# Optimization experiments

Measured on AMD Instinct MI355X. Metric: run time of the kernel, lower is better.

Reference implementation:

```python
import jax, jax.numpy as jnp
import numpy as np

N, C, P, M = 8, 20, 8732, 16
THRESHOLD, NEG_POS_RATIO, ALPHA = 0.5, 3, 1.0


def cxcy_to_xy(c):
    return jnp.concatenate([c[..., :2] - c[..., 2:] / 2.0, c[..., :2] + c[..., 2:] / 2.0], axis=-1)


def xy_to_cxcy(xy):
    return jnp.concatenate([(xy[..., :2] + xy[..., 2:]) / 2.0, xy[..., 2:] - xy[..., :2]], axis=-1)


def cxcy_to_gcxgcy(cxcy, priors):
    g_cxcy = (cxcy[..., :2] - priors[..., :2]) / (priors[..., 2:] / 10.0)
    g_wh = jnp.log(cxcy[..., 2:] / priors[..., 2:]) * 5.0
    return jnp.concatenate([g_cxcy, g_wh], axis=-1)


def jaccard(a, b):
    # a: (M,4), b: (P,4), boundary coords -> IoU (M,P)
    lo = jnp.maximum(a[:, None, :2], b[None, :, :2])
    hi = jnp.minimum(a[:, None, 2:], b[None, :, 2:])
    inter = jnp.prod(jnp.clip(hi - lo, 0.0), axis=-1)
    area_a = jnp.prod(a[:, 2:] - a[:, :2], axis=-1)
    area_b = jnp.prod(b[:, 2:] - b[:, :2], axis=-1)
    return inter / (area_a[:, None] + area_b[None, :] - inter)


def setup_inputs() -> dict:
    key = jax.random.key(0)
    k1, k2, k3, k4, k5, k6 = jax.random.split(key, 6)
    predicted_locs = jax.random.normal(k1, (N, C, P, 4), jnp.float32)
    predicted_scores = jax.random.normal(k2, (N, C, P, 2), jnp.float32)
    # valid ground-truth boundary boxes (x1<x2, y1<y2) in [0,1]
    ctr = jax.random.uniform(k3, (N, C, M, 2), minval=0.2, maxval=0.8)
    wh = jax.random.uniform(k4, (N, C, M, 2), minval=0.05, maxval=0.3)
    boxes = jnp.concatenate([ctr - wh / 2.0, ctr + wh / 2.0], axis=-1)
    # valid priors in cxcywh (w,h > 0 so log-encoding is finite)
    pctr = jax.random.uniform(k5, (P, 2), minval=0.05, maxval=0.95)
    pwh = jax.random.uniform(k6, (P, 2), minval=0.05, maxval=0.5)
    priors_cxcy = jnp.concatenate([pctr, pwh], axis=-1)
    labels = jnp.ones((N, C, M), jnp.int32)  # binary per-class head: object label = 1
    return {
        "predicted_locs": predicted_locs,
        "predicted_scores": predicted_scores,
        "boxes": boxes,
        "labels": labels,
        "priors_cxcy": priors_cxcy,
    }


def _forward(predicted_locs, predicted_scores, boxes, priors_cxcy, labels):
    n_classes = predicted_scores.shape[1]
    n_priors = predicted_scores.shape[2]
    priors_xy = cxcy_to_xy(priors_cxcy)

    def match(b, lab):
        # b: (M,4) boundary, lab: (M,) int
        ov = jaccard(b, priors_xy)                       # (M,P)
        obj_for_prior = jnp.argmax(ov, axis=0)           # (P,)
        ov_for_prior = jnp.max(ov, axis=0)               # (P,)
        prior_for_obj = jnp.argmax(ov, axis=1)           # (M,)
        # force each object to own its best prior
        obj_for_prior = obj_for_prior.at[prior_for_obj].set(jnp.arange(b.shape[0]))
        ov_for_prior = ov_for_prior.at[prior_for_obj].set(1.0)
        cls = jnp.where(ov_for_prior < THRESHOLD, 0, lab[obj_for_prior])  # (P,)
        tl = cxcy_to_gcxgcy(xy_to_cxcy(b[obj_for_prior]), priors_cxcy)    # (P,4)
        return tl, cls

    true_locs, true_classes = jax.vmap(jax.vmap(match))(boxes, labels)  # (N,C,P,4), (N,C,P)

    pos = true_classes != 0                      # (N,C,P)
    posf = pos.astype(predicted_locs.dtype)
    n_pos_bc = posf.sum(axis=2)                  # (N,C) positives per image per class
    n_pos_c = n_pos_bc.sum(axis=0)               # (C,)

    # localization: mean L1 over positive priors (4 coords each), per class
    l1 = jnp.abs(predicted_locs - true_locs).sum(-1) * posf   # (N,C,P)
    loc_loss_c = l1.sum(axis=(0, 2)) / jnp.maximum(n_pos_c * 4.0, 1.0)

    # per-prior binary cross entropy
    logp = jax.nn.log_softmax(predicted_scores, axis=-1)      # (N,C,P,2)
    ce = -jnp.take_along_axis(logp, true_classes[..., None], axis=-1)[..., 0]  # (N,C,P)
    conf_pos_c = (ce * posf).sum(axis=(0, 2))

    # hard negative mining: sort negatives desc per (image,class) row, keep top 3*n_pos
    ce_neg = jnp.where(pos, 0.0, ce)
    ce_neg_sorted = -jnp.sort(-ce_neg, axis=-1)               # (N,C,P) descending
    n_hard = NEG_POS_RATIO * n_pos_bc                         # (N,C)
    ranks = jnp.arange(n_priors, dtype=n_hard.dtype)
    hard_mask = ranks[None, None, :] < n_hard[..., None]
    conf_hard_c = (ce_neg_sorted * hard_mask).sum(axis=(0, 2))

    safe = jnp.maximum(n_pos_c, 1.0)
    loss_c = jnp.where(
        n_pos_c > 0,
        (conf_pos_c + conf_hard_c + ALPHA * loc_loss_c) / safe,
        0.0,
    ) / n_classes
    return loss_c.sum()


def reference(predicted_locs, predicted_scores, boxes, labels, priors_cxcy):
    return _forward(predicted_locs, predicted_scores, boxes, priors_cxcy, labels)
```

## Files before the change

### kernel.cpp

```cpp
#include <hip/hip_runtime.h>
#include <math.h>

#define NN 8
#define CC 20
#define PP 8732
#define MM 16
#define NPR 3
#define SPLIT 8
#define CH 1092
#define ROWS (NN * CC)

__device__ __forceinline__ float fast_rcp(float x) { return __builtin_amdgcn_rcpf(x); }

__device__ __forceinline__ float lse2(float a, float b) {
    float mx = fmaxf(a, b);
    float d  = fabsf(a - b);
    return mx + logf(1.0f + expf(-d));
}

#define ABLK 256
__global__ __launch_bounds__(ABLK) void mbox_p1(
    const float* __restrict__ locs, const float* __restrict__ scores,
    const float* __restrict__ boxes, const int* __restrict__ labels,
    const float* __restrict__ priors,
    unsigned char* __restrict__ pk8, float* __restrict__ ce0,
    unsigned long long* __restrict__ partials, float* __restrict__ cstats)
{
    const int row = blockIdx.x >> 3;
    const int chunk = blockIdx.x & 7;
    const int tid = threadIdx.x, lane = tid & 63, wav = tid >> 6;
    __shared__ float s_bx1[MM], s_by1[MM], s_bx2[MM], s_by2[MM], s_area[MM];
    __shared__ float s_bcx[MM], s_bcy[MM], s_bw[MM], s_bh[MM];
    __shared__ int s_lab[MM];
    __shared__ unsigned long long s_pk[4 * MM];
    __shared__ float s_rf[4 * 3];

    if (tid < MM) {
        const float* b = boxes + ((size_t)row * MM + tid) * 4;
        float x1 = b[0], y1 = b[1], x2 = b[2], y2 = b[3];
        s_bx1[tid] = x1; s_by1[tid] = y1; s_bx2[tid] = x2; s_by2[tid] = y2;
        s_area[tid] = (x2 - x1) * (y2 - y1);
        s_bcx[tid] = (x1 + x2) * 0.5f; s_bcy[tid] = (y1 + y2) * 0.5f;
        s_bw[tid] = x2 - x1; s_bh[tid] = y2 - y1;
        s_lab[tid] = labels[row * MM + tid];
    }
    __syncthreads();

    const float4* pri4 = (const float4*)priors;
    const float4* loc4 = (const float4*)(locs + (size_t)row * PP * 4);
    const float2* sc2  = (const float2*)(scores + (size_t)row * PP * 2);
    unsigned char* pk  = pk8 + (size_t)row * PP;
    float* cer         = ce0 + (size_t)row * PP;

    float bestv[MM]; int bestp[MM];
#pragma unroll
    for (int m = 0; m < MM; m++) { bestv[m] = -1.0f; bestp[m] = 0x7fffffff; }
    float l_np = 0.0f, l_l1 = 0.0f, l_cp = 0.0f;
    const int p0 = chunk * CH, p1e = min(p0 + CH, PP);

    for (int p = p0 + tid; p < p1e; p += ABLK) {
        float4 pr = pri4[p];
        float hw = pr.z * 0.5f, hh = pr.w * 0.5f;
        float px1 = pr.x - hw, py1 = pr.y - hh;
        float px2 = pr.x + hw, py2 = pr.y + hh;
        float area_b = (px2 - px1) * (py2 - py1);
        float bov = -1.0f; int bm = 0;
#pragma unroll
        for (int m = 0; m < MM; m++) {
            float dx = fminf(s_bx2[m], px2) - fmaxf(s_bx1[m], px1);
            float dy = fminf(s_by2[m], py2) - fmaxf(s_by1[m], py1);
            dx = fmaxf(dx, 0.0f); dy = fmaxf(dy, 0.0f);
            float inter = dx * dy;
            float den = s_area[m] + area_b - inter;
            float iou = inter * fast_rcp(den);
            if (iou > bov) { bov = iou; bm = m; }
            if (iou > bestv[m]) { bestv[m] = iou; bestp[m] = p; }
        }
        float2 sc = sc2[p];
        float lse = lse2(sc.x, sc.y);
        bool pos = (bov >= 0.5f) && (s_lab[bm] != 0);
        pk[p]  = (unsigned char)((pos ? 16u : 0u) | (unsigned)bm);
        cer[p] = pos ? 0.0f : fmaxf(lse - sc.x, 0.0f);
        if (pos) {
            l_np += 1.0f;
            l_cp += lse - sc.y;
            float4 pl = loc4[p];
            float tx = (s_bcx[bm] - pr.x) * 10.0f / pr.z;
            float ty = (s_bcy[bm] - pr.y) * 10.0f / pr.w;
            float tw = logf(s_bw[bm] / pr.z) * 5.0f;
            float th = logf(s_bh[bm] / pr.w) * 5.0f;
            l_l1 += fabsf(pl.x - tx) + fabsf(pl.y - ty) + fabsf(pl.z - tw) + fabsf(pl.w - th);
        }
    }

#pragma unroll
    for (int m = 0; m < MM; m++) {
        unsigned long long key =
            ((unsigned long long)__float_as_uint(bestv[m]) << 32) |
            (unsigned)(0x7fffffff - bestp[m]);
#pragma unroll
        for (int off = 32; off; off >>= 1) {
            unsigned long long o = __shfl_down(key, off);
            if (o > key) key = o;
        }
        if (lane == 0) s_pk[wav * MM + m] = key;
    }
#pragma unroll
    for (int off = 32; off; off >>= 1) {
        l_np += __shfl_down(l_np, off);
        l_l1 += __shfl_down(l_l1, off);
        l_cp += __shfl_down(l_cp, off);
    }
    if (lane == 0) { s_rf[wav * 3] = l_np; s_rf[wav * 3 + 1] = l_l1; s_rf[wav * 3 + 2] = l_cp; }
    __syncthreads();
    if (tid < MM) {
        unsigned long long key = s_pk[tid];
        for (int w = 1; w < 4; w++) {
            unsigned long long o = s_pk[w * MM + tid];
            if (o > key) key = o;
        }
        partials[((size_t)row * MM + tid) * SPLIT + chunk] = key;
    }
    if (tid == 0) {
        float np = 0, l1 = 0, cp = 0;
        for (int w = 0; w < 4; w++) { np += s_rf[w * 3]; l1 += s_rf[w * 3 + 1]; cp += s_rf[w * 3 + 2]; }
        float* cs = cstats + ((size_t)row * SPLIT + chunk) * 3;
        cs[0] = np; cs[1] = l1; cs[2] = cp;
    }
}

#define CBLK 1024
#define EPT 9
__global__ __launch_bounds__(CBLK) void mbox_sel(
    const float* __restrict__ locs, const float* __restrict__ scores,
    const float* __restrict__ boxes, const int* __restrict__ labels,
    const float* __restrict__ priors,
    const unsigned char* __restrict__ pk8, const float* __restrict__ ce0,
    const unsigned long long* __restrict__ partials,
    const float* __restrict__ cstats, float* __restrict__ rstats)
{
    const int row = blockIdx.x, tid = threadIdx.x, lane = tid & 63, wav = tid >> 6;
    __shared__ float s_bcx[MM], s_bcy[MM], s_bw[MM], s_bh[MM];
    __shared__ int s_lab[MM], s_pfo[MM], s_fp[MM];
    __shared__ float s_fv[MM], s_sum[3];
    __shared__ unsigned int s_cnt[16][4];
    __shared__ unsigned int s_K;
    __shared__ float s_redf[16];
    __shared__ int s_redi[16];

    if (tid < 64) ((unsigned int*)s_cnt)[tid] = 0u;
    if (tid < MM) {
        s_fp[tid] = -1;
        const float* b = boxes + ((size_t)row * MM + tid) * 4;
        float x1 = b[0], y1 = b[1], x2 = b[2], y2 = b[3];
        s_bcx[tid] = (x1 + x2) * 0.5f; s_bcy[tid] = (y1 + y2) * 0.5f;
        s_bw[tid] = x2 - x1; s_bh[tid] = y2 - y1;
        s_lab[tid] = labels[row * MM + tid];
        const unsigned long long* pr = partials + ((size_t)row * MM + tid) * SPLIT;
        unsigned long long key = pr[0];
        for (int c = 1; c < SPLIT; c++) { unsigned long long o = pr[c]; if (o > key) key = o; }
        s_pfo[tid] = 0x7fffffff - (int)(unsigned)(key & 0xffffffffull);
    }
    if (tid >= 16 && tid < 19) {
        int j = tid - 16; float s = 0;
        for (int c = 0; c < SPLIT; c++) s += cstats[((size_t)row * SPLIT + c) * 3 + j];
        s_sum[j] = s;
    }
    __syncthreads();

    float d_np = 0, d_l1 = 0, d_cp = 0;
    if (tid < MM) {
        int p = s_pfo[tid];
        bool is_last = true;
        for (int mm = tid + 1; mm < MM; mm++) if (s_pfo[mm] == p) is_last = false;
        if (is_last) {
            const float4 pr = ((const float4*)priors)[p];
            const float4 pl = ((const float4*)(locs + (size_t)row * PP * 4))[p];
            const float2 sc = ((const float2*)(scores + (size_t)row * PP * 2))[p];
            float lse = lse2(sc.x, sc.y);
            unsigned int u = pk8[(size_t)row * PP + p];
            if (u & 16u) {
                int mo = u & 15;
                d_np -= 1.0f; d_cp -= (lse - sc.y);
                float tx = (s_bcx[mo] - pr.x) * 10.0f / pr.z;
                float ty = (s_bcy[mo] - pr.y) * 10.0f / pr.w;
                float tw = logf(s_bw[mo] / pr.z) * 5.0f;
                float th = logf(s_bh[mo] / pr.w) * 5.0f;
                d_l1 -= fabsf(pl.x - tx) + fabsf(pl.y - ty) + fabsf(pl.z - tw) + fabsf(pl.w - th);
            }
            if (s_lab[tid] != 0) {
                d_np += 1.0f; d_cp += (lse - sc.y);
                float tx = (s_bcx[tid] - pr.x) * 10.0f / pr.z;
                float ty = (s_bcy[tid] - pr.y) * 10.0f / pr.w;
                float tw = logf(s_bw[tid] / pr.z) * 5.0f;
                float th = logf(s_bh[tid] / pr.w) * 5.0f;
                d_l1 += fabsf(pl.x - tx) + fabsf(pl.y - ty) + fabsf(pl.z - tw) + fabsf(pl.w - th);
                s_fv[tid] = 0.0f;
            } else {
                s_fv[tid] = fmaxf(lse - sc.x, 0.0f);
            }
            s_fp[tid] = p;
        }
    }
    if (tid < 64) {
#pragma unroll
        for (int off = 32; off; off >>= 1) {
            d_np += __shfl_down(d_np, off);
            d_l1 += __shfl_down(d_l1, off);
            d_cp += __shfl_down(d_cp, off);
        }
        if (tid == 0) {
            float np = s_sum[0] + d_np;
            rstats[(size_t)row * 8 + 0] = np;
            rstats[(size_t)row * 8 + 1] = s_sum[1] + d_l1;
            rstats[(size_t)row * 8 + 2] = s_sum[2] + d_cp;
            int K = NPR * (int)(np + 0.5f);
            s_K = (K > 0) ? (unsigned)K : 0u;
        }
    }
    __syncthreads();

    const float* cer = ce0 + (size_t)row * PP;
    unsigned int uv[EPT];
#pragma unroll
    for (int k = 0; k < EPT; k++) {
        int p = tid + k * CBLK;
        uv[k] = (p < PP) ? __float_as_uint(cer[p]) : 0u;
    }
    for (int t = 0; t < MM; t++) {
        int fp = s_fp[t];
        if (fp >= 0) {
            unsigned int fb = __float_as_uint(s_fv[t]);
#pragma unroll
            for (int k = 0; k < EPT; k++) if (tid + k * CBLK == fp) uv[k] = fb;
        }
    }

    const unsigned int K = s_K;
    unsigned int T = 0u;
    if (K > 0u) {
        for (int r = 0; r < 16; r++) {
            const int b = 30 - 2 * r;
            const unsigned int T1 = T | (1u << b), T2 = T | (2u << b), T3 = T | (3u << b);
            unsigned int c1 = 0, c2 = 0, c3 = 0;
#pragma unroll
            for (int k = 0; k < EPT; k++) {
                unsigned int u = uv[k];
                c1 += (u >= T1); c2 += (u >= T2); c3 += (u >= T3);
            }
#pragma unroll
            for (int off = 32; off; off >>= 1) {
                c1 += __shfl_down(c1, off);
                c2 += __shfl_down(c2, off);
                c3 += __shfl_down(c3, off);
            }
            if (lane == 0) {
                atomicAdd(&s_cnt[r][1], c1);
                atomicAdd(&s_cnt[r][2], c2);
                atomicAdd(&s_cnt[r][3], c3);
            }
            __syncthreads();
            unsigned int C1 = s_cnt[r][1], C2 = s_cnt[r][2], C3 = s_cnt[r][3];
            if      (C3 >= K) T = T3;
            else if (C2 >= K) T = T2;
            else if (C1 >= K) T = T1;
        }
    }

    float sgt = 0.0f; int cgt = 0;
    if (K > 0u) {
#pragma unroll
        for (int k = 0; k < EPT; k++) {
            unsigned int u = uv[k];
            if (u > T) { sgt += __uint_as_float(u); cgt++; }
        }
    }
#pragma unroll
    for (int off = 32; off; off >>= 1) {
        sgt += __shfl_down(sgt, off);
        cgt += __shfl_down(cgt, off);
    }
    if (lane == 0) { s_redf[wav] = sgt; s_redi[wav] = cgt; }
    __syncthreads();
    if (tid == 0) {
        float s = 0; int cnt = 0;
        for (int w = 0; w < 16; w++) { s += s_redf[w]; cnt += s_redi[w]; }
        float chard = (K > 0u) ? (s + (float)(int)(K - (unsigned)cnt) * __uint_as_float(T)) : 0.0f;
        rstats[(size_t)row * 8 + 4] = chard;
    }
}

__global__ void mbox_finalize(const float* __restrict__ rstats, float* __restrict__ out) {
    int c = threadIdx.x;
    float loss = 0.0f;
    if (c < CC) {
        float np = 0, l1 = 0, cp = 0, ch = 0;
        for (int n = 0; n < NN; n++) {
            const float* s = rstats + ((size_t)(n * CC + c)) * 8;
            np += s[0]; l1 += s[1]; cp += s[2]; ch += s[4];
        }
        float loc = l1 / fmaxf(np * 4.0f, 1.0f);
        float val = (np > 0.0f) ? (cp + ch + loc) / fmaxf(np, 1.0f) : 0.0f;
        loss = val / (float)CC;
    }
#pragma unroll
    for (int off = 32; off; off >>= 1) loss += __shfl_down(loss, off);
    if (threadIdx.x == 0) out[0] = loss;
}

extern "C" void kernel_launch(void* const* d_in, const int* in_sizes, int n_in,
                              void* d_out, int out_size, void* d_ws, size_t ws_size,
                              hipStream_t stream) {
    const float* locs   = (const float*)d_in[0];
    const float* scores = (const float*)d_in[1];
    const float* boxes  = (const float*)d_in[2];
    const int*   labels = (const int*)d_in[3];
    const float* priors = (const float*)d_in[4];
    float* out = (float*)d_out;

    char* ws = (char*)d_ws;
    float* ce0                   = (float*)ws;
    unsigned char* pk8           = (unsigned char*)(ws + 5588480);
    unsigned long long* partials = (unsigned long long*)(ws + 6985600);
    float* cstats                = (float*)(ws + 7149440);
    float* rstats                = (float*)(ws + 7164800);

    mbox_p1<<<ROWS * SPLIT, ABLK, 0, stream>>>(locs, scores, boxes, labels, priors,
                                               pk8, ce0, partials, cstats);
    mbox_sel<<<ROWS, CBLK, 0, stream>>>(locs, scores, boxes, labels, priors,
                                        pk8, ce0, partials, cstats, rstats);
    mbox_finalize<<<1, 64, 0, stream>>>(rstats, out);
}
```

Measured before the change: 149.9 us.

## Recompute negative CE in selection kernel instead of storing ce0 buffer

```diff
diff --git a/kernel.cpp b/kernel.cpp
--- a/kernel.cpp
+++ b/kernel.cpp
@@ -15,7 +15,7 @@
 __device__ __forceinline__ float lse2(float a, float b) {
     float mx = fmaxf(a, b);
     float d  = fabsf(a - b);
-    return mx + logf(1.0f + expf(-d));
+    return mx + __logf(1.0f + __expf(-d));
 }
 
 #define ABLK 256
@@ -23,26 +23,36 @@
     const float* __restrict__ locs, const float* __restrict__ scores,
     const float* __restrict__ boxes, const int* __restrict__ labels,
     const float* __restrict__ priors,
-    unsigned char* __restrict__ pk8, float* __restrict__ ce0,
+    unsigned char* __restrict__ pk8,
     unsigned long long* __restrict__ partials, float* __restrict__ cstats)
 {
     const int row = blockIdx.x >> 3;
     const int chunk = blockIdx.x & 7;
     const int tid = threadIdx.x, lane = tid & 63, wav = tid >> 6;
-    __shared__ float s_bx1[MM], s_by1[MM], s_bx2[MM], s_by2[MM], s_area[MM];
+
     __shared__ float s_bcx[MM], s_bcy[MM], s_bw[MM], s_bh[MM];
-    __shared__ int s_lab[MM];
     __shared__ unsigned long long s_pk[4 * MM];
     __shared__ float s_rf[4 * 3];
 
+    float bx1[MM], by1[MM], bx2[MM], by2[MM], bar[MM];
+    unsigned int labm = 0;
+    {
+        const float* bb = boxes + (size_t)row * MM * 4;
+        const int*   lb = labels + (size_t)row * MM;
+#pragma unroll
+        for (int m = 0; m < MM; m++) {
+            float x1 = bb[m * 4 + 0], y1 = bb[m * 4 + 1];
+            float x2 = bb[m * 4 + 2], y2 = bb[m * 4 + 3];
+            bx1[m] = x1; by1[m] = y1; bx2[m] = x2; by2[m] = y2;
+            bar[m] = (x2 - x1) * (y2 - y1);
+            labm |= (lb[m] != 0 ? 1u : 0u) << m;
+        }
+    }
     if (tid < MM) {
-        const float* b = boxes + ((size_t)row * MM + tid) * 4;
-        float x1 = b[0], y1 = b[1], x2 = b[2], y2 = b[3];
-        s_bx1[tid] = x1; s_by1[tid] = y1; s_bx2[tid] = x2; s_by2[tid] = y2;
-        s_area[tid] = (x2 - x1) * (y2 - y1);
-        s_bcx[tid] = (x1 + x2) * 0.5f; s_bcy[tid] = (y1 + y2) * 0.5f;
-        s_bw[tid] = x2 - x1; s_bh[tid] = y2 - y1;
-        s_lab[tid] = labels[row * MM + tid];
+        s_bcx[tid] = (bx1[tid] + bx2[tid]) * 0.5f;
+        s_bcy[tid] = (by1[tid] + by2[tid]) * 0.5f;
+        s_bw[tid]  = bx2[tid] - bx1[tid];
+        s_bh[tid]  = by2[tid] - by1[tid];
     }
     __syncthreads();
 
@@ -50,7 +60,6 @@
     const float4* loc4 = (const float4*)(locs + (size_t)row * PP * 4);
     const float2* sc2  = (const float2*)(scores + (size_t)row * PP * 2);
     unsigned char* pk  = pk8 + (size_t)row * PP;
-    float* cer         = ce0 + (size_t)row * PP;
 
     float bestv[MM]; int bestp[MM];
 #pragma unroll
@@ -58,6 +67,7 @@
     float l_np = 0.0f, l_l1 = 0.0f, l_cp = 0.0f;
     const int p0 = chunk * CH, p1e = min(p0 + CH, PP);
 
+#pragma unroll 2
     for (int p = p0 + tid; p < p1e; p += ABLK) {
         float4 pr = pri4[p];
         float hw = pr.z * 0.5f, hh = pr.w * 0.5f;
@@ -67,28 +77,26 @@
         float bov = -1.0f; int bm = 0;
 #pragma unroll
         for (int m = 0; m < MM; m++) {
-            float dx = fminf(s_bx2[m], px2) - fmaxf(s_bx1[m], px1);
-            float dy = fminf(s_by2[m], py2) - fmaxf(s_by1[m], py1);
+            float dx = fminf(bx2[m], px2) - fmaxf(bx1[m], px1);
+            float dy = fminf(by2[m], py2) - fmaxf(by1[m], py1);
             dx = fmaxf(dx, 0.0f); dy = fmaxf(dy, 0.0f);
             float inter = dx * dy;
-            float den = s_area[m] + area_b - inter;
+            float den = bar[m] + area_b - inter;
             float iou = inter * fast_rcp(den);
             if (iou > bov) { bov = iou; bm = m; }
             if (iou > bestv[m]) { bestv[m] = iou; bestp[m] = p; }
         }
-        float2 sc = sc2[p];
-        float lse = lse2(sc.x, sc.y);
-        bool pos = (bov >= 0.5f) && (s_lab[bm] != 0);
-        pk[p]  = (unsigned char)((pos ? 16u : 0u) | (unsigned)bm);
-        cer[p] = pos ? 0.0f : fmaxf(lse - sc.x, 0.0f);
+        bool pos = (bov >= 0.5f) && (((labm >> bm) & 1u) != 0u);
+        pk[p] = (unsigned char)((pos ? 16u : 0u) | (unsigned)bm);
         if (pos) {
+            float2 sc = sc2[p];
+            float4 pl = loc4[p];
             l_np += 1.0f;
-            l_cp += lse - sc.y;
-            float4 pl = loc4[p];
+            l_cp += lse2(sc.x, sc.y) - sc.y;
             float tx = (s_bcx[bm] - pr.x) * 10.0f / pr.z;
             float ty = (s_bcy[bm] - pr.y) * 10.0f / pr.w;
-            float tw = logf(s_bw[bm] / pr.z) * 5.0f;
-            float th = logf(s_bh[bm] / pr.w) * 5.0f;
+            float tw = __logf(s_bw[bm] / pr.z) * 5.0f;
+            float th = __logf(s_bh[bm] / pr.w) * 5.0f;
             l_l1 += fabsf(pl.x - tx) + fabsf(pl.y - ty) + fabsf(pl.z - tw) + fabsf(pl.w - th);
         }
     }
@@ -135,7 +143,7 @@
     const float* __restrict__ locs, const float* __restrict__ scores,
     const float* __restrict__ boxes, const int* __restrict__ labels,
     const float* __restrict__ priors,
-    const unsigned char* __restrict__ pk8, const float* __restrict__ ce0,
+    const unsigned char* __restrict__ pk8,
     const unsigned long long* __restrict__ partials,
     const float* __restrict__ cstats, float* __restrict__ rstats)
 {
@@ -184,16 +192,16 @@
                 d_np -= 1.0f; d_cp -= (lse - sc.y);
                 float tx = (s_bcx[mo] - pr.x) * 10.0f / pr.z;
                 float ty = (s_bcy[mo] - pr.y) * 10.0f / pr.w;
-                float tw = logf(s_bw[mo] / pr.z) * 5.0f;
-                float th = logf(s_bh[mo] / pr.w) * 5.0f;
+                float tw = __logf(s_bw[mo] / pr.z) * 5.0f;
+                float th = __logf(s_bh[mo] / pr.w) * 5.0f;
                 d_l1 -= fabsf(pl.x - tx) + fabsf(pl.y - ty) + fabsf(pl.z - tw) + fabsf(pl.w - th);
             }
             if (s_lab[tid] != 0) {
                 d_np += 1.0f; d_cp += (lse - sc.y);
                 float tx = (s_bcx[tid] - pr.x) * 10.0f / pr.z;
                 float ty = (s_bcy[tid] - pr.y) * 10.0f / pr.w;
-                float tw = logf(s_bw[tid] / pr.z) * 5.0f;
-                float th = logf(s_bh[tid] / pr.w) * 5.0f;
+                float tw = __logf(s_bw[tid] / pr.z) * 5.0f;
+                float th = __logf(s_bh[tid] / pr.w) * 5.0f;
                 d_l1 += fabsf(pl.x - tx) + fabsf(pl.y - ty) + fabsf(pl.z - tw) + fabsf(pl.w - th);
                 s_fv[tid] = 0.0f;
             } else {
@@ -220,12 +228,18 @@
     }
     __syncthreads();
 
-    const float* cer = ce0 + (size_t)row * PP;
+    const float2* sc2 = (const float2*)(scores + (size_t)row * PP * 2);
+    const unsigned char* pk = pk8 + (size_t)row * PP;
     unsigned int uv[EPT];
 #pragma unroll
     for (int k = 0; k < EPT; k++) {
         int p = tid + k * CBLK;
-        uv[k] = (p < PP) ? __float_as_uint(cer[p]) : 0u;
+        if (p < PP) {
+            unsigned int u8 = pk[p];
+            float2 sc = sc2[p];
+            float ce = (u8 & 16u) ? 0.0f : fmaxf(lse2(sc.x, sc.y) - sc.x, 0.0f);
+            uv[k] = __float_as_uint(ce);
+        } else uv[k] = 0u;
     }
     for (int t = 0; t < MM; t++) {
         int fp = s_fp[t];
@@ -319,15 +333,14 @@
     float* out = (float*)d_out;
 
     char* ws = (char*)d_ws;
-    float* ce0                   = (float*)ws;
-    unsigned char* pk8           = (unsigned char*)(ws + 5588480);
-    unsigned long long* partials = (unsigned long long*)(ws + 6985600);
-    float* cstats                = (float*)(ws + 7149440);
-    float* rstats                = (float*)(ws + 7164800);
+    unsigned char* pk8           = (unsigned char*)ws;
+    unsigned long long* partials = (unsigned long long*)(ws + 1397120);
+    float* cstats                = (float*)(ws + 1560960);
+    float* rstats                = (float*)(ws + 1576320);
 
     mbox_p1<<<ROWS * SPLIT, ABLK, 0, stream>>>(locs, scores, boxes, labels, priors,
-                                               pk8, ce0, partials, cstats);
+                                               pk8, partials, cstats);
     mbox_sel<<<ROWS, CBLK, 0, stream>>>(locs, scores, boxes, labels, priors,
-                                        pk8, ce0, partials, cstats, rstats);
+                                        pk8, partials, cstats, rstats);
     mbox_finalize<<<1, 64, 0, stream>>>(rstats, out);
 }
```

Result: no change. 150.3 us (+0.3%).
